# Kernel optimization log

Measured on AMD Instinct MI355X. Metric: run time of the kernel, lower is better.

## Reference

```python
import jax, jax.numpy as jnp
import numpy as np

WIDTH = 64
KER_W = 128
DEPTH = 4
N_NODES = 10000

def _lin(x, w, b):
    return x @ w.T + b

def _kernel_mlp(ea, w1, b1, w2, b2, w3, b3):
    # DenseNet([ker_in, 64, 128, 64*64], ReLU): ReLU between layers, none after last
    h = jax.nn.relu(_lin(ea, w1, b1))
    h = jax.nn.relu(_lin(h, w2, b2))
    return _lin(h, w3, b3)

def _nnconv(x, edge_index, edge_attr, w1, b1, w2, b2, w3, b3, root, bias):
    E = edge_attr.shape[0]
    W = _kernel_mlp(edge_attr, w1, b1, w2, b2, w3, b3).reshape(E, WIDTH, WIDTH)  # [E,in,out]
    src, dst = edge_index[0], edge_index[1]
    msg = jnp.einsum('ei,eio->eo', x[src], W)                     # gather + per-edge matmul
    s = jax.ops.segment_sum(msg, dst, num_segments=N_NODES)
    cnt = jax.ops.segment_sum(jnp.ones((E,), x.dtype), dst, num_segments=N_NODES)
    agg = s / jnp.maximum(cnt, 1.0)[:, None]                      # scatter-mean (empty -> 0)
    return agg + x @ root + bias

def setup_inputs() -> dict:
    key = jax.random.key(0)
    ks = jax.random.split(key, 32)
    N, E, Eb, KIN = N_NODES, 20000, 4000, 6
    d = {}
    d['x'] = jax.random.normal(ks[0], (N, 1), jnp.float32)
    d['edge_index'] = jax.random.randint(ks[1], (2, E), 0, N)
    d['edge_attr'] = jax.random.uniform(ks[2], (E, KIN), jnp.float32)
    d['edge_index_boundary'] = jax.random.randint(ks[3], (2, Eb), 0, N)
    d['edge_attr_boundary'] = jax.random.uniform(ks[4], (Eb, KIN), jnp.float32)
    def lin_p(k, fout, fin):
        k1, k2 = jax.random.split(k)
        sc = 1.0 / np.sqrt(fin)
        return (jax.random.uniform(k1, (fout, fin), jnp.float32, -sc, sc),
                jax.random.uniform(k2, (fout,), jnp.float32, -sc, sc))
    d['fc1_w'], d['fc1_b'] = lin_p(ks[5], WIDTH, 1)
    d['fc2_w'], d['fc2_b'] = lin_p(ks[6], KER_W, WIDTH)
    d['fc3_w'], d['fc3_b'] = lin_p(ks[7], 1, KER_W)
    # kernel 1 (interior edges)
    d['k1_w1'], d['k1_b1'] = lin_p(ks[8], KER_W // 2, KIN)
    d['k1_w2'], d['k1_b2'] = lin_p(ks[9], KER_W, KER_W // 2)
    d['k1_w3'], d['k1_b3'] = lin_p(ks[10], WIDTH * WIDTH, KER_W)
    d['root1'] = jax.random.uniform(ks[11], (WIDTH, WIDTH), jnp.float32, -0.1, 0.1)
    d['bias1'] = jax.random.uniform(ks[12], (WIDTH,), jnp.float32, -0.1, 0.1)
    # kernel 2 (boundary edges)
    d['k2_w1'], d['k2_b1'] = lin_p(ks[13], KER_W // 2, KIN)
    d['k2_w2'], d['k2_b2'] = lin_p(ks[14], KER_W, KER_W // 2)
    d['k2_w3'], d['k2_b3'] = lin_p(ks[15], WIDTH * WIDTH, KER_W)
    d['root2'] = jax.random.uniform(ks[16], (WIDTH, WIDTH), jnp.float32, -0.1, 0.1)
    d['bias2'] = jax.random.uniform(ks[17], (WIDTH,), jnp.float32, -0.1, 0.1)
    return d

def reference(x, edge_index, edge_attr, edge_index_boundary, edge_attr_boundary,
              fc1_w, fc1_b, fc2_w, fc2_b, fc3_w, fc3_b,
              k1_w1, k1_b1, k1_w2, k1_b2, k1_w3, k1_b3, root1, bias1,
              k2_w1, k2_b1, k2_w2, k2_b2, k2_w3, k2_b3, root2, bias2):
    x0 = _lin(x, fc1_w, fc1_b)   # fc1(data.x), reused every layer
    h = x0
    for _ in range(DEPTH):
        h = (_nnconv(h, edge_index, edge_attr, k1_w1, k1_b1, k1_w2, k1_b2, k1_w3, k1_b3, root1, bias1)
             + _nnconv(h, edge_index_boundary, edge_attr_boundary, k2_w1, k2_b1, k2_w2, k2_b2, k2_w3, k2_b3, root2, bias2))
        h = jax.nn.relu(h) + x0
    h = jax.nn.relu(_lin(h, fc2_w, fc2_b))
    return _lin(h, fc3_w, fc3_b)
```

## Files before the change

### kernel.cpp

```cpp
#include <hip/hip_runtime.h>
#include <hip/hip_bf16.h>

typedef unsigned short u16;
typedef unsigned int u32;
typedef unsigned long long u64;

#define WIDTH 64
#define KERW 4096
#define K2DIM 128
#define DEPTH 4
#define MEB 16

typedef __attribute__((ext_vector_type(8))) short short8;
typedef __attribute__((ext_vector_type(4))) float f32x4;
typedef __attribute__((ext_vector_type(4))) u32 u32x4;
typedef __attribute__((ext_vector_type(4))) u16 u16x4;

__device__ __forceinline__ u16 f2bf(float f) {
    union { float f; u32 u; } v; v.f = f;
    u32 r = v.u + 0x7FFFu + ((v.u >> 16) & 1u);
    return (u16)(r >> 16);
}
__device__ __forceinline__ float bflo(u32 u) { return __uint_as_float(u << 16); }
__device__ __forceinline__ float bfhi(u32 u) { return __uint_as_float(u & 0xFFFF0000u); }


__global__ void pre_k(const int* __restrict__ dst1, int E,
                      const int* __restrict__ dst2, int Eb,
                      float* __restrict__ cnt, int N,
                      const float* __restrict__ x, const float* __restrict__ fc1w,
                      const float* __restrict__ fc1b, float* __restrict__ x0,
                      const float* __restrict__ w3a, const float* __restrict__ b3a,
                      u16* __restrict__ Bp1, float* __restrict__ b3p1,
                      const float* __restrict__ w3b, const float* __restrict__ b3b,
                      u16* __restrict__ Bp2, float* __restrict__ b3p2,
                      int nbC, int nbF) {
    int bid = blockIdx.x, t = threadIdx.x;
    if (bid < nbC) {
        int i = bid * 256 + t;
        if (i < E) atomicAdd(&cnt[dst1[i]], 1.0f);
        else if (i < E + Eb) atomicAdd(&cnt[N + dst2[i - E]], 1.0f);
        return;
    }
    bid -= nbC;
    if (bid < nbF) {
        int idx = bid * 256 + t;
        if (idx < N * WIDTH) {
            int n = idx >> 6, j = idx & 63;
            x0[idx] = fc1w[j] * x[n] + fc1b[j];
        }
        return;
    }
    bid -= nbF;
    const float* w3 = w3a; const float* b3 = b3a;
    u16* Bp = Bp1; float* b3p = b3p1;
    if (bid >= 2048) { bid -= 2048; w3 = w3b; b3 = b3b; Bp = Bp2; b3p = b3p2; }
    int idx = bid * 256 + t;
    int c = idx >> 7, k = idx & 127;
    int i = c & 63, o = c >> 6;
    int pr = (i << 6) | o;
    size_t w = (size_t)(c >> 4) * 2048 + (k >> 5) * 512
             + (((c & 15) + 16 * ((k >> 3) & 3)) << 3) + (k & 7);
    Bp[w] = f2bf(w3[(size_t)pr * 128 + k]);
    if (k == 0) b3p[(o << 6) | ((i & 15) << 2) | (i >> 4)] = b3[pr];
}

__global__ __launch_bounds__(256) void mlp12_k(const float* __restrict__ eaA,
                                               const float* __restrict__ w1A, const float* __restrict__ b1A,
                                               const float* __restrict__ w2A, const float* __restrict__ b2A,
                                               u16* __restrict__ h2A, int EA, int nbA,
                                               const float* __restrict__ eaB,
                                               const float* __restrict__ w1B, const float* __restrict__ b1B,
                                               const float* __restrict__ w2B, const float* __restrict__ b2B,
                                               u16* __restrict__ h2B, int EB) {
    __shared__ u16   w2b[64 * 136];
    __shared__ float h1s[MEB * 65];
    __shared__ float w1s[64 * 6];
    __shared__ float b1s[64];
    __shared__ float b2s[128];
    __shared__ float eas[MEB * 6];
    int bid = blockIdx.x, t = threadIdx.x;
    const float *ea, *w1, *b1, *w2, *b2; u16* h2p; int E, e0;
    if (bid < nbA) { ea = eaA; w1 = w1A; b1 = b1A; w2 = w2A; b2 = b2A; h2p = h2A; E = EA; e0 = bid * MEB; }
    else { ea = eaB; w1 = w1B; b1 = b1B; w2 = w2B; b2 = b2B; h2p = h2B; E = EB; e0 = (bid - nbA) * MEB; }
    for (int i = t; i < 8192; i += 256)
        w2b[(i & 63) * 136 + (i >> 6)] = f2bf(w2[i]);
    for (int i = t; i < 384; i += 256) w1s[i] = w1[i];
    if (t < 64) b1s[t] = b1[t];
    if (t < 128) b2s[t] = b2[t];
    {
        int ne = min(MEB, E - e0) * 6;
        if (t < ne) eas[t] = ea[(size_t)e0 * 6 + t];
    }
    __syncthreads();
    for (int id = t; id < MEB * 64; id += 256) {
        int el = id >> 6, o = id & 63;
        float a = b1s[o];
        #pragma unroll
        for (int k = 0; k < 6; ++k) a += eas[el * 6 + k] * w1s[o * 6 + k];
        h1s[el * 65 + o] = fmaxf(a, 0.f);
    }
    __syncthreads();
    int el = t >> 4, og = (t & 15) * 8;
    int e = e0 + el;
    float acc[8];
    #pragma unroll
    for (int c = 0; c < 8; ++c) acc[c] = b2s[og + c];
    const float* h1r = &h1s[el * 65];
    #pragma unroll 8
    for (int j = 0; j < 64; ++j) {
        float hj = h1r[j];
        uint4 v = *(const uint4*)&w2b[j * 136 + og];
        acc[0] += bflo(v.x) * hj; acc[1] += bfhi(v.x) * hj;
        acc[2] += bflo(v.y) * hj; acc[3] += bfhi(v.y) * hj;
        acc[4] += bflo(v.z) * hj; acc[5] += bfhi(v.z) * hj;
        acc[6] += bflo(v.w) * hj; acc[7] += bfhi(v.w) * hj;
    }
    if (e < E) {
        size_t idx = (size_t)(e >> 4) * 2048 + (og >> 5) * 512
                   + (((e & 15) + 16 * ((og >> 3) & 3)) << 3);
        ushort4 p0, p1;
        p0.x = f2bf(fmaxf(acc[0], 0.f)); p0.y = f2bf(fmaxf(acc[1], 0.f));
        p0.z = f2bf(fmaxf(acc[2], 0.f)); p0.w = f2bf(fmaxf(acc[3], 0.f));
        p1.x = f2bf(fmaxf(acc[4], 0.f)); p1.y = f2bf(fmaxf(acc[5], 0.f));
        p1.z = f2bf(fmaxf(acc[6], 0.f)); p1.w = f2bf(fmaxf(acc[7], 0.f));
        *(ushort4*)(h2p + idx)     = p0;
        *(ushort4*)(h2p + idx + 4) = p1;
    }
}

__global__ __launch_bounds__(256, 4) void w3_mfma_k(const u16* __restrict__ h2A,
                                                    const u16* __restrict__ BpA,
                                                    const float* __restrict__ b3pA,
                                                    u16* __restrict__ WtA, int EA, int nEA, int g1,
                                                    const u16* __restrict__ h2B,
                                                    const u16* __restrict__ BpB,
                                                    const float* __restrict__ b3pB,
                                                    u16* __restrict__ WtB, int EB, int nEB) {
    int p = blockIdx.x;
    const u16 *h2p, *Bp; const float* b3p; u16* Wt; int E, nE;
    if (p < g1) { h2p = h2A; Bp = BpA; b3p = b3pA; Wt = WtA; E = EA; nE = nEA; }
    else { p -= g1; h2p = h2B; Bp = BpB; b3p = b3pB; Wt = WtB; E = EB; nE = nEB; }
    int xcd = p & 7, j = p >> 3;
    int t = (j >> 5) * 8 + xcd;
    if (t >= nE) return;
    int eb = t << 7, cb = (j & 31) << 7;

    int lane = threadIdx.x & 63, wv = threadIdx.x >> 6;
    int wr = (wv >> 1) << 6, wc = (wv & 1) << 6;
    int lr = lane & 15, lg = lane >> 4;

    const u16* abase = h2p + (size_t)((eb + wr) >> 4) * 2048 + lane * 8;
    const u16* bbase = Bp  + (size_t)((cb + wc) >> 4) * 2048 + lane * 8;

    f32x4 acc[4][4] = {};
    #pragma unroll
    for (int kk = 0; kk < 4; ++kk) {
        short8 af[4], bf[4];
        #pragma unroll
        for (int m = 0; m < 4; ++m) af[m] = *(const short8*)(abase + m * 2048 + kk * 512);
        #pragma unroll
        for (int n = 0; n < 4; ++n) bf[n] = *(const short8*)(bbase + n * 2048 + kk * 512);
        #pragma unroll
        for (int m = 0; m < 4; ++m)
            #pragma unroll
            for (int n = 0; n < 4; ++n)
                acc[m][n] = __builtin_amdgcn_mfma_f32_16x16x32_bf16(af[m], bf[n], acc[m][n], 0, 0, 0);
    }

    float4 bb4 = *(const float4*)(b3p + cb + wc + lr * 4);

    #pragma unroll
    for (int m = 0; m < 4; ++m) {
        #pragma unroll
        for (int r4 = 0; r4 < 4; ++r4) {
            int eg = eb + wr + m * 16 + lg * 4 + r4;
            if (eg < E) {
                u16x4 pk;
                pk[0] = f2bf(acc[m][0][r4] + bb4.x);
                pk[1] = f2bf(acc[m][1][r4] + bb4.y);
                pk[2] = f2bf(acc[m][2][r4] + bb4.z);
                pk[3] = f2bf(acc[m][3][r4] + bb4.w);
                __builtin_nontemporal_store(pk, (u16x4*)(Wt + (size_t)eg * KERW + cb + wc + lr * 4));
            }
        }
    }
}

__global__ __launch_bounds__(256) void msg_k(const float* __restrict__ h,
                                             const u16* __restrict__ WtA,
                                             const int* __restrict__ srcA, const int* __restrict__ dstA,
                                             float* __restrict__ sA, int EA, int nbA,
                                             const u16* __restrict__ WtB,
                                             const int* __restrict__ srcB, const int* __restrict__ dstB,
                                             float* __restrict__ sB, int EB) {
    __shared__ float hs[4][64];
    int bid = blockIdx.x;
    int w = threadIdx.x >> 6, l = threadIdx.x & 63;
    const u16* Wt; const int *src, *dst; float* s; int E, e;
    if (bid < nbA) { Wt = WtA; src = srcA; dst = dstA; s = sA; E = EA; e = bid * 4 + w; }
    else { Wt = WtB; src = srcB; dst = dstB; s = sB; E = EB; e = (bid - nbA) * 4 + w; }
    bool valid = e < E;
    int ec = valid ? e : 0;
    int sv = src[ec];
    hs[w][((l & 15) << 2) | (l >> 4)] = h[(size_t)sv * 64 + l];
    __syncthreads();
    float4 h0 = *(const float4*)&hs[w][(l & 7) * 8];
    float4 h1 = *(const float4*)&hs[w][(l & 7) * 8 + 4];
    const char* base = (const char*)(Wt + (size_t)ec * KERW) + l * 16;
    float acc[8];
    #pragma unroll
    for (int jj = 0; jj < 8; ++jj) {
        u32x4 v = __builtin_nontemporal_load((const u32x4*)(base + jj * 1024));
        float a;
        a  = bflo(v[0]) * h0.x; a += bfhi(v[0]) * h0.y;
        a += bflo(v[1]) * h0.z; a += bfhi(v[1]) * h0.w;
        a += bflo(v[2]) * h1.x; a += bfhi(v[2]) * h1.y;
        a += bflo(v[3]) * h1.z; a += bfhi(v[3]) * h1.w;
        acc[jj] = a;
    }
    #pragma unroll
    for (int jj = 0; jj < 8; ++jj) {
        acc[jj] += __shfl_xor(acc[jj], 1, 64);
        acc[jj] += __shfl_xor(acc[jj], 2, 64);
        acc[jj] += __shfl_xor(acc[jj], 4, 64);
    }
    int c = l & 7;
    float val = acc[0];
    #pragma unroll
    for (int jj = 1; jj < 8; ++jj) val = (c == jj) ? acc[jj] : val;
    if (valid) atomicAdd(&s[(size_t)dst[ec] * 64 + ((c << 3) | (l >> 3))], val);
}

__global__ __launch_bounds__(256) void combine_k(const float* __restrict__ h,
                                                 float* __restrict__ s,
                                                 const float* __restrict__ cnt,
                                                 const float* __restrict__ root1, const float* __restrict__ root2,
                                                 const float* __restrict__ bias1, const float* __restrict__ bias2,
                                                 const float* __restrict__ x0, float* __restrict__ hout, int N) {
    __shared__ float rs[64][64];
    __shared__ float hr[4][64];
    int t = threadIdx.x;
    for (int j = t; j < 4096; j += 256) rs[j >> 6][j & 63] = root1[j] + root2[j];
    int w = t >> 6, o = t & 63;
    float bsum = bias1[o] + bias2[o];
    __syncthreads();
    #pragma unroll
    for (int g = 0; g < 4; ++g) {
        int n = blockIdx.x * 16 + g * 4 + w;
        bool valid = n < N;
        int nc = valid ? n : 0;
        hr[w][o] = h[(size_t)nc * 64 + o];
        float inv1 = 1.0f / fmaxf(cnt[nc], 1.0f);
        float inv2 = 1.0f / fmaxf(cnt[N + nc], 1.0f);
        float acc = s[(size_t)nc * 64 + o] * inv1
                  + s[(size_t)(N + nc) * 64 + o] * inv2
                  + bsum;
        if (valid) {
            s[(size_t)nc * 64 + o] = 0.f;
            s[(size_t)(N + nc) * 64 + o] = 0.f;
        }
        #pragma unroll 8
        for (int i = 0; i < 64; ++i) acc += hr[w][i] * rs[i][o];
        if (valid) hout[(size_t)n * 64 + o] = fmaxf(acc, 0.f) + x0[(size_t)n * 64 + o];
    }
}

__global__ __launch_bounds__(128) void head_k(const float* __restrict__ h,
                                              const float* __restrict__ fc2w, const float* __restrict__ fc2b,
                                              const float* __restrict__ fc3w, const float* __restrict__ fc3b,
                                              float* __restrict__ out, int N) {
    __shared__ float hr[64];
    __shared__ float red[128];
    int n = blockIdx.x, t = threadIdx.x;
    if (t < 64) hr[t] = h[(size_t)n * 64 + t];
    __syncthreads();
    float a = fc2b[t];
    #pragma unroll 8
    for (int i = 0; i < 64; ++i) a += hr[i] * fc2w[t * 64 + i];
    red[t] = fmaxf(a, 0.f) * fc3w[t];
    __syncthreads();
    if (t < 64) {
        float v = red[t] + red[t + 64];
        for (int off = 32; off; off >>= 1) v += __shfl_down(v, off);
        if (t == 0) out[n] = v + fc3b[0];
    }
}

extern "C" void kernel_launch(void* const* d_in, const int* in_sizes, int n_in,
                              void* d_out, int out_size, void* d_ws, size_t ws_size,
                              hipStream_t stream) {
    const float* x    = (const float*)d_in[0];
    const int*   ei   = (const int*)d_in[1];
    const float* ea   = (const float*)d_in[2];
    const int*   eib  = (const int*)d_in[3];
    const float* eab  = (const float*)d_in[4];
    const float* fc1w = (const float*)d_in[5];
    const float* fc1b = (const float*)d_in[6];
    const float* fc2w = (const float*)d_in[7];
    const float* fc2b = (const float*)d_in[8];
    const float* fc3w = (const float*)d_in[9];
    const float* fc3b = (const float*)d_in[10];
    const float* k1w1 = (const float*)d_in[11];
    const float* k1b1 = (const float*)d_in[12];
    const float* k1w2 = (const float*)d_in[13];
    const float* k1b2 = (const float*)d_in[14];
    const float* k1w3 = (const float*)d_in[15];
    const float* k1b3 = (const float*)d_in[16];
    const float* root1 = (const float*)d_in[17];
    const float* bias1 = (const float*)d_in[18];
    const float* k2w1 = (const float*)d_in[19];
    const float* k2b1 = (const float*)d_in[20];
    const float* k2w2 = (const float*)d_in[21];
    const float* k2b2 = (const float*)d_in[22];
    const float* k2w3 = (const float*)d_in[23];
    const float* k2b3 = (const float*)d_in[24];
    const float* root2 = (const float*)d_in[25];
    const float* bias2 = (const float*)d_in[26];
    float* out = (float*)d_out;

    const int N  = in_sizes[0];
    const int E  = in_sizes[2] / 6;
    const int Eb = in_sizes[4] / 6;

    const int nE1 = (E + 127) / 128,  nE1p = ((nE1 + 7) / 8) * 8;
    const int nE2 = (Eb + 127) / 128, nE2p = ((nE2 + 7) / 8) * 8;

    char* p = (char*)d_ws;
    auto alloc = [&](size_t bytes) {
        char* r = p;
        p += (bytes + 255) & ~(size_t)255;
        return (void*)r;
    };
    float* x0   = (float*)alloc((size_t)N * 64 * 4);
    float* hA   = (float*)alloc((size_t)N * 64 * 4);
    float* hB   = (float*)alloc((size_t)N * 64 * 4);
    float* sbuf = (float*)alloc((size_t)2 * N * 64 * 4);
    float* cnt  = (float*)alloc((size_t)2 * N * 4);
    char*  zero0 = (char*)sbuf;
    size_t zero0Bytes = (size_t)((char*)cnt - (char*)sbuf) + (size_t)2 * N * 4;
    size_t h2aBytes = (size_t)nE1p * 128 * K2DIM * 2;
    size_t h2bBytes = (size_t)nE2p * 128 * K2DIM * 2;
    u16*   h2a  = (u16*)alloc(h2aBytes);
    u16*   h2b  = (u16*)alloc(h2bBytes);
    size_t zero1Bytes = (size_t)((char*)h2b - (char*)h2a) + h2bBytes;
    u16*   Bp1  = (u16*)alloc((size_t)KERW * K2DIM * 2);
    u16*   Bp2  = (u16*)alloc((size_t)KERW * K2DIM * 2);
    float* b3p1 = (float*)alloc((size_t)KERW * 4);
    float* b3p2 = (float*)alloc((size_t)KERW * 4);
    u16*   W1   = (u16*)alloc((size_t)E * KERW * 2);
    u16*   W2   = (u16*)alloc((size_t)Eb * KERW * 2);
    (void)ws_size;

    const int* src1 = ei;       const int* dst1 = ei + E;
    const int* src2 = eib;      const int* dst2 = eib + Eb;

    hipMemsetAsync(zero0, 0, zero0Bytes, stream);
    hipMemsetAsync(h2a, 0, zero1Bytes, stream);

    {
        int nbA = (E + MEB - 1) / MEB, nbB = (Eb + MEB - 1) / MEB;
        mlp12_k<<<nbA + nbB, 256, 0, stream>>>(ea, k1w1, k1b1, k1w2, k1b2, h2a, E, nbA,
                                               eab, k2w1, k2b1, k2w2, k2b2, h2b, Eb);
    }
    {
        int nbC = (E + Eb + 255) / 256;
        int nbF = (N * WIDTH + 255) / 256;
        pre_k<<<nbC + nbF + 4096, 256, 0, stream>>>(dst1, E, dst2, Eb, cnt, N,
                                                    x, fc1w, fc1b, x0,
                                                    k1w3, k1b3, Bp1, b3p1,
                                                    k2w3, k2b3, Bp2, b3p2,
                                                    nbC, nbF);
    }
    {
        int g1 = nE1p * 32, g2 = nE2p * 32;
        w3_mfma_k<<<g1 + g2, 256, 0, stream>>>(h2a, Bp1, b3p1, W1, E, nE1, g1,
                                               h2b, Bp2, b3p2, W2, Eb, nE2);
    }

    const float* hcur = x0;
    float* bufs[2] = { hA, hB };
    int nbM1 = (E + 3) / 4, nbM2 = (Eb + 3) / 4;
    for (int l = 0; l < DEPTH; ++l) {
        float* hnext = bufs[l & 1];
        msg_k<<<nbM1 + nbM2, 256, 0, stream>>>(hcur, W1, src1, dst1, sbuf, E, nbM1,
                                               W2, src2, dst2, sbuf + (size_t)N * 64, Eb);
        combine_k<<<(N + 15) / 16, 256, 0, stream>>>(hcur, sbuf, cnt, root1, root2, bias1, bias2,
                                                     x0, hnext, N);
        hcur = hnext;
    }

    head_k<<<N, 128, 0, stream>>>(hcur, fc2w, fc2b, fc3w, fc3b, out, N);
}
```

Baseline: 307.9 us.

## Fuse first-layer message computation into the edge-weight GEMM epilogue

```diff
diff --git a/kernel.cpp b/kernel.cpp
--- a/kernel.cpp
+++ b/kernel.cpp
@@ -133,22 +133,41 @@
                                                     const u16* __restrict__ BpA,
                                                     const float* __restrict__ b3pA,
                                                     u16* __restrict__ WtA, int EA, int nEA, int g1,
+                                                    const int* __restrict__ srcA, const int* __restrict__ dstA,
+                                                    float* __restrict__ sA,
                                                     const u16* __restrict__ h2B,
                                                     const u16* __restrict__ BpB,
                                                     const float* __restrict__ b3pB,
-                                                    u16* __restrict__ WtB, int EB, int nEB) {
+                                                    u16* __restrict__ WtB, int EB, int nEB,
+                                                    const int* __restrict__ srcB, const int* __restrict__ dstB,
+                                                    float* __restrict__ sB,
+                                                    const float* __restrict__ x0) {
+    __shared__ float x0s[128][68];
     int p = blockIdx.x;
     const u16 *h2p, *Bp; const float* b3p; u16* Wt; int E, nE;
-    if (p < g1) { h2p = h2A; Bp = BpA; b3p = b3pA; Wt = WtA; E = EA; nE = nEA; }
-    else { p -= g1; h2p = h2B; Bp = BpB; b3p = b3pB; Wt = WtB; E = EB; nE = nEB; }
+    const int *src, *dst; float* s;
+    if (p < g1) { h2p = h2A; Bp = BpA; b3p = b3pA; Wt = WtA; E = EA; nE = nEA; src = srcA; dst = dstA; s = sA; }
+    else { p -= g1; h2p = h2B; Bp = BpB; b3p = b3pB; Wt = WtB; E = EB; nE = nEB; src = srcB; dst = dstB; s = sB; }
     int xcd = p & 7, j = p >> 3;
     int t = (j >> 5) * 8 + xcd;
     if (t >= nE) return;
     int eb = t << 7, cb = (j & 31) << 7;
 
-    int lane = threadIdx.x & 63, wv = threadIdx.x >> 6;
+    int tid = threadIdx.x;
+    int lane = tid & 63, wv = tid >> 6;
     int wr = (wv >> 1) << 6, wc = (wv & 1) << 6;
     int lr = lane & 15, lg = lane >> 4;
+
+    {
+        int row = tid >> 1, half = tid & 1;
+        int eg = eb + row;
+        int ec = (eg < E) ? eg : 0;
+        const float4* xr = (const float4*)(x0 + (size_t)src[ec] * 64 + half * 32);
+        float4* dstp = (float4*)&x0s[row][half * 32];
+        #pragma unroll
+        for (int q = 0; q < 8; ++q) dstp[q] = xr[q];
+    }
+    __syncthreads();
 
     const u16* abase = h2p + (size_t)((eb + wr) >> 4) * 2048 + lane * 8;
     const u16* bbase = Bp  + (size_t)((cb + wc) >> 4) * 2048 + lane * 8;
@@ -169,19 +188,31 @@
     }
 
     float4 bb4 = *(const float4*)(b3p + cb + wc + lr * 4);
+    int o = (cb + wc) >> 6;
 
     #pragma unroll
     for (int m = 0; m < 4; ++m) {
         #pragma unroll
         for (int r4 = 0; r4 < 4; ++r4) {
-            int eg = eb + wr + m * 16 + lg * 4 + r4;
+            int egl = wr + m * 16 + lg * 4 + r4;
+            int eg = eb + egl;
+            float w0 = acc[m][0][r4] + bb4.x;
+            float w1 = acc[m][1][r4] + bb4.y;
+            float w2 = acc[m][2][r4] + bb4.z;
+            float w3 = acc[m][3][r4] + bb4.w;
+            float pmsg = w0 * x0s[egl][lr]
+                       + w1 * x0s[egl][16 + lr]
+                       + w2 * x0s[egl][32 + lr]
+                       + w3 * x0s[egl][48 + lr];
+            pmsg += __shfl_xor(pmsg, 1, 64);
+            pmsg += __shfl_xor(pmsg, 2, 64);
+            pmsg += __shfl_xor(pmsg, 4, 64);
+            pmsg += __shfl_xor(pmsg, 8, 64);
             if (eg < E) {
                 u16x4 pk;
-                pk[0] = f2bf(acc[m][0][r4] + bb4.x);
-                pk[1] = f2bf(acc[m][1][r4] + bb4.y);
-                pk[2] = f2bf(acc[m][2][r4] + bb4.z);
-                pk[3] = f2bf(acc[m][3][r4] + bb4.w);
+                pk[0] = f2bf(w0); pk[1] = f2bf(w1); pk[2] = f2bf(w2); pk[3] = f2bf(w3);
                 __builtin_nontemporal_store(pk, (u16x4*)(Wt + (size_t)eg * KERW + cb + wc + lr * 4));
+                if (lr == 0) atomicAdd(&s[(size_t)dst[eg] * 64 + o], pmsg);
             }
         }
     }
@@ -375,7 +406,10 @@
     {
         int g1 = nE1p * 32, g2 = nE2p * 32;
         w3_mfma_k<<<g1 + g2, 256, 0, stream>>>(h2a, Bp1, b3p1, W1, E, nE1, g1,
-                                               h2b, Bp2, b3p2, W2, Eb, nE2);
+                                               src1, dst1, sbuf,
+                                               h2b, Bp2, b3p2, W2, Eb, nE2,
+                                               src2, dst2, sbuf + (size_t)N * 64,
+                                               x0);
     }
 
     const float* hcur = x0;
@@ -383,8 +417,10 @@
     int nbM1 = (E + 3) / 4, nbM2 = (Eb + 3) / 4;
     for (int l = 0; l < DEPTH; ++l) {
         float* hnext = bufs[l & 1];
-        msg_k<<<nbM1 + nbM2, 256, 0, stream>>>(hcur, W1, src1, dst1, sbuf, E, nbM1,
-                                               W2, src2, dst2, sbuf + (size_t)N * 64, Eb);
+        if (l > 0) {
+            msg_k<<<nbM1 + nbM2, 256, 0, stream>>>(hcur, W1, src1, dst1, sbuf, E, nbM1,
+                                                   W2, src2, dst2, sbuf + (size_t)N * 64, Eb);
+        }
         combine_k<<<(N + 15) / 16, 256, 0, stream>>>(hcur, sbuf, cnt, root1, root2, bias1, bias2,
                                                      x0, hnext, N);
         hcur = hnext;
```

Result: slower. 363.2 us (+17.9%).
